# Performance work log

Hardware: AMD Instinct MI355X
Metric: run time of the kernel (lower is better)

Reference implementation:

```python
import jax, jax.numpy as jnp
import numpy as np
import math

B, S, E, H = 2, 2048, 1024, 16
D = E // H
EPS = 1e-5


def setup_inputs() -> dict:
    key = jax.random.key(0)
    ks = jax.random.split(key, 6)
    s = 1.0 / math.sqrt(E)
    return {
        "query": jax.random.normal(ks[0], (B, S, E), jnp.float32),
        "Wq": jax.random.normal(ks[1], (E, E), jnp.float32) * s,
        "bq": jnp.zeros((E,), jnp.float32),
        "Wk": jax.random.normal(ks[2], (E, E), jnp.float32) * s,
        "bk": jnp.zeros((E,), jnp.float32),
        "Wv": jax.random.normal(ks[3], (E, E), jnp.float32) * s,
        "bv": jnp.zeros((E,), jnp.float32),
        "Wo": jax.random.normal(ks[4], (E, E), jnp.float32) * s,
        "bo": jnp.zeros((E,), jnp.float32),
        "alpha": jnp.ones((1,), jnp.float32),
    }


def reference(query, Wq, bq, Wk, bk, Wv, bv, Wo, bo, alpha):
    # Q/K/V projections (nn.Linear: x @ W.T + b)
    q = (query @ Wq.T + bq).reshape(B, S, H, D)
    k = (query @ Wk.T + bk).reshape(B, S, H, D)
    v = (query @ Wv.T + bv).reshape(B, S, H, D)

    # YAT scores: (q.k)^2 / (||q-k||^2 + eps)
    qk = jnp.einsum('bqhd,bkhd->bhqk', q, k)          # [B,H,S,S]
    sq = jnp.einsum('bqhd,bqhd->bhq', q, q)           # ||q||^2
    sk = jnp.einsum('bkhd,bkhd->bhk', k, k)           # ||k||^2
    dist_sq = sq[..., :, None] + sk[..., None, :] - 2.0 * qk
    scores = (qk * qk) / (dist_sq + EPS)

    # learnable alpha scaling: scores * (sqrt(d)/log(1+d))^alpha
    scale = (jnp.sqrt(jnp.float32(D)) / jnp.log1p(jnp.float32(D))) ** alpha[0]
    scores = scores * scale

    attn = jax.nn.softmax(scores, axis=-1)
    out = jnp.einsum('bhqk,bkhd->bqhd', attn, v).reshape(B, S, E)
    return out @ Wo.T + bo
```

## Files before the change

### kernel.cpp

```cpp
#include <hip/hip_runtime.h>
#include <math.h>

#define BB 2
#define SS 2048
#define EE 1024
#define HH 16
#define DD 64
#define YAT_EPS 1e-5f

typedef __attribute__((ext_vector_type(8))) short bf16x8;
typedef __attribute__((ext_vector_type(4))) short short4v;
typedef __attribute__((ext_vector_type(4))) float f32x4;
typedef __attribute__((ext_vector_type(2))) float f32x2;
#define MFMA16(a, b, c) __builtin_amdgcn_mfma_f32_16x16x32_bf16((a), (b), (c), 0, 0, 0)

#if __has_builtin(__builtin_amdgcn_exp2f)
#define EXP2(x) __builtin_amdgcn_exp2f(x)
#else
#define EXP2(x) exp2f(x)
#endif
#if __has_builtin(__builtin_amdgcn_rcpf)
#define RCPF(x) __builtin_amdgcn_rcpf(x)
#else
#define RCPF(x) (1.0f / (x))
#endif

__device__ __forceinline__ unsigned short f2bf(float x) {
    unsigned int u = __float_as_uint(x);
    u += 0x7FFFu + ((u >> 16) & 1u);
    return (unsigned short)(u >> 16);
}
__device__ __forceinline__ float bf2f(unsigned short h) {
    return __uint_as_float(((unsigned int)h) << 16);
}
__device__ __forceinline__ short f2bf_t(float x) {
    return (short)(__float_as_uint(x) >> 16);
}

__device__ __forceinline__ void async_ld16(void* lds, const void* g) {
    __builtin_amdgcn_global_load_lds(
        (const __attribute__((address_space(1))) unsigned int*)g,
        (__attribute__((address_space(3))) unsigned int*)lds, 16, 0, 0);
}

__global__ __launch_bounds__(256) void split_f32(const float* __restrict__ in,
                                                 unsigned short* __restrict__ hi,
                                                 unsigned short* __restrict__ lo,
                                                 int n4) {
    int i = blockIdx.x * 256 + threadIdx.x;
    if (i >= n4) return;
    float4 v = ((const float4*)in)[i];
    ushort4 h, l;
    h.x = f2bf(v.x); l.x = f2bf(v.x - bf2f(h.x));
    h.y = f2bf(v.y); l.y = f2bf(v.y - bf2f(h.y));
    h.z = f2bf(v.z); l.z = f2bf(v.z - bf2f(h.z));
    h.w = f2bf(v.w); l.w = f2bf(v.w - bf2f(h.w));
    ((ushort4*)hi)[i] = h;
    ((ushort4*)lo)[i] = l;
}

__global__ __launch_bounds__(256) void split_w4(
        const float* __restrict__ Wq, const float* __restrict__ Wk,
        const float* __restrict__ Wv, const float* __restrict__ Wo,
        unsigned short* __restrict__ Whi, unsigned short* __restrict__ Wlo,
        unsigned short* __restrict__ Wohi) {
    int i = blockIdx.x * 256 + threadIdx.x;
    int y = blockIdx.y;
    const float* src = y == 0 ? Wq : y == 1 ? Wk : y == 2 ? Wv : Wo;
    unsigned short* hi = y < 3 ? Whi + (size_t)y * EE * EE : Wohi;
    float4 v = ((const float4*)src)[i];
    ushort4 h;
    h.x = f2bf(v.x); h.y = f2bf(v.y); h.z = f2bf(v.z); h.w = f2bf(v.w);
    ((ushort4*)hi)[i] = h;
    if (y < 2) {
        unsigned short* lo = Wlo + (size_t)y * EE * EE;
        ushort4 l;
        l.x = f2bf(v.x - bf2f(h.x));
        l.y = f2bf(v.y - bf2f(h.y));
        l.z = f2bf(v.z - bf2f(h.z));
        l.w = f2bf(v.w - bf2f(h.w));
        ((ushort4*)lo)[i] = l;
    }
}

template <int MODE, int PASSES>
__global__ __launch_bounds__(256, 2) void gemm3p(
        const unsigned short* __restrict__ Ahi, const unsigned short* __restrict__ Alo,
        const unsigned short* __restrict__ Bhi, const unsigned short* __restrict__ Blo,
        const float* __restrict__ bq, const float* __restrict__ bk,
        const float* __restrict__ bv,
        float* __restrict__ Cf,
        unsigned short* __restrict__ qhi, unsigned short* __restrict__ qlo,
        unsigned short* __restrict__ khi,
        unsigned short* __restrict__ v_sd,
        float* __restrict__ sqn, float* __restrict__ skn,
        int M, int N, int K) {
    __shared__ __align__(16) unsigned short LA_hi[128 * 32];
    __shared__ __align__(16) unsigned short LA_lo[128 * 32];
    __shared__ __align__(16) unsigned short LB_hi[128 * 32];
    __shared__ __align__(16) unsigned short LB_lo[128 * 32];

    const int t = threadIdx.x;
    const int w = t >> 6, lane = t & 63;
    const int quad = lane >> 4, lr = lane & 15;
    const int wy = w & 1, wx = w >> 1;
    const int m0 = blockIdx.y * 128, n0 = blockIdx.x * 128;

    const unsigned short* gsrc = nullptr;
    unsigned short* ldst = nullptr;
    if (w == 0)      { gsrc = Ahi + (size_t)m0 * K; ldst = LA_hi; }
    else if (w == 2) { gsrc = Bhi + (size_t)n0 * K; ldst = LB_hi; }
    else if (PASSES == 3 && w == 1) { gsrc = Alo + (size_t)m0 * K; ldst = LA_lo; }
    else if (PASSES == 3 && w == 3) { gsrc = Blo + (size_t)n0 * K; ldst = LB_lo; }
    const unsigned short* gl = gsrc ? gsrc + (size_t)(lane >> 2) * K + (lane & 3) * 8
                                    : nullptr;

    f32x4 acc[4][4];
    #pragma unroll
    for (int i = 0; i < 4; ++i)
        #pragma unroll
        for (int j = 0; j < 4; ++j)
            acc[i][j] = (f32x4){0.f, 0.f, 0.f, 0.f};

    for (int k0 = 0; k0 < K; k0 += 32) {
        __syncthreads();
        if (gl) {
            #pragma unroll
            for (int i = 0; i < 8; ++i)
                async_ld16(ldst + i * 512, gl + (size_t)i * 16 * K + k0);
        }
        __syncthreads();
        bf16x8 ah[4], al[4], bh_[4], bl_[4];
        #pragma unroll
        for (int i = 0; i < 4; ++i) {
            ah[i]  = *(const bf16x8*)&LA_hi[(wy * 64 + i * 16 + lr) * 32 + quad * 8];
            bh_[i] = *(const bf16x8*)&LB_hi[(wx * 64 + i * 16 + lr) * 32 + quad * 8];
            if (PASSES == 3) {
                al[i]  = *(const bf16x8*)&LA_lo[(wy * 64 + i * 16 + lr) * 32 + quad * 8];
                bl_[i] = *(const bf16x8*)&LB_lo[(wx * 64 + i * 16 + lr) * 32 + quad * 8];
            }
        }
        #pragma unroll
        for (int mg = 0; mg < 4; ++mg)
            #pragma unroll
            for (int ns = 0; ns < 4; ++ns) {
                f32x4 a = acc[mg][ns];
                a = MFMA16(ah[mg], bh_[ns], a);
                if (PASSES == 3) {
                    a = MFMA16(ah[mg], bl_[ns], a);
                    a = MFMA16(al[mg], bh_[ns], a);
                }
                acc[mg][ns] = a;
            }
    }

    const int ng = n0 + wx * 64;
    if (MODE == 0) {
        float bias_v[4];
        #pragma unroll
        for (int ns = 0; ns < 4; ++ns) bias_v[ns] = bq[ng + ns * 16 + lr];
        #pragma unroll
        for (int mg = 0; mg < 4; ++mg)
            #pragma unroll
            for (int r = 0; r < 4; ++r) {
                int m = m0 + wy * 64 + mg * 16 + quad * 4 + r;
                #pragma unroll
                for (int ns = 0; ns < 4; ++ns)
                    Cf[(size_t)m * N + ng + ns * 16 + lr] = acc[mg][ns][r] + bias_v[ns];
            }
    } else {
        const int path = MODE == 1 ? (ng >> 10) : 2;
        const int c = MODE == 1 ? (ng & 1023) : ng;
        const int h = c >> 6;
        const float* bias = path == 0 ? bq : path == 1 ? bk : bv;
        unsigned short* hi_p = path == 0 ? qhi : path == 1 ? khi : v_sd;
        float* nrm = path == 0 ? sqn : skn;
        float bias_v[4];
        #pragma unroll
        for (int ns = 0; ns < 4; ++ns) bias_v[ns] = bias[c + ns * 16 + lr];
        #pragma unroll
        for (int mg = 0; mg < 4; ++mg)
            #pragma unroll
            for (int r = 0; r < 4; ++r) {
                int m = m0 + wy * 64 + mg * 16 + quad * 4 + r;
                int b = m >> 11, s = m & (SS - 1);
                size_t base = ((size_t)(b * HH + h) * SS + s) * DD;
                float v4[4];
                #pragma unroll
                for (int ns = 0; ns < 4; ++ns) v4[ns] = acc[mg][ns][r] + bias_v[ns];
                if (path < 2) {
                    float pn = v4[0] * v4[0] + v4[1] * v4[1] + v4[2] * v4[2] + v4[3] * v4[3];
                    #pragma unroll
                    for (int off = 1; off < 16; off <<= 1) pn += __shfl_xor(pn, off);
                    if (lr == 0) nrm[(size_t)(b * HH + h) * SS + s] = pn;
                    #pragma unroll
                    for (int ns = 0; ns < 4; ++ns) {
                        unsigned short hv = f2bf(v4[ns]);
                        hi_p[base + ns * 16 + lr] = hv;
                        if (path == 0)
                            qlo[base + ns * 16 + lr] = f2bf(v4[ns] - bf2f(hv));
                    }
                } else {
                    #pragma unroll
                    for (int ns = 0; ns < 4; ++ns)
                        hi_p[base + ns * 16 + lr] = f2bf(v4[ns]);
                }
            }
    }
}

__global__ __launch_bounds__(256) void transpose_v(const unsigned short* __restrict__ v_sd,
                                                   unsigned short* __restrict__ vt) {
    __shared__ unsigned short T[64][65];
    const int t = threadIdx.x;
    const int bh = blockIdx.y, s0 = blockIdx.x * 64;
    {
        int sl = t >> 2, d4 = (t & 3) * 16;
        const unsigned short* src = &v_sd[((size_t)bh * SS + s0 + sl) * DD + d4];
        bf16x8 a = *(const bf16x8*)src;
        bf16x8 b = *(const bf16x8*)(src + 8);
        #pragma unroll
        for (int j = 0; j < 8; ++j) {
            T[sl][d4 + j] = (unsigned short)a[j];
            T[sl][d4 + 8 + j] = (unsigned short)b[j];
        }
    }
    __syncthreads();
    {
        int dl = t >> 2, s4 = (t & 3) * 16;
        bf16x8 a, b;
        #pragma unroll
        for (int j = 0; j < 8; ++j) {
            a[j] = (short)T[s4 + j][dl];
            b[j] = (short)T[s4 + 8 + j][dl];
        }
        unsigned short* dst = &vt[((size_t)bh * DD + dl) * SS + s0 + s4];
        *(bf16x8*)dst = a;
        *(bf16x8*)(dst + 8) = b;
    }
}

__global__ __launch_bounds__(256, 3) void yat_attn_mfma(
        const unsigned short* __restrict__ qhi, const unsigned short* __restrict__ qlo,
        const unsigned short* __restrict__ khi,
        const unsigned short* __restrict__ vt,
        const float* __restrict__ sqn, const float* __restrict__ skn,
        const float* __restrict__ alphap,
        unsigned short* __restrict__ ctxhi) {
    __shared__ __align__(16) unsigned short Ks[2][4096];
    __shared__ __align__(16) unsigned short Ps[2][4][16 * 68];

    const int t = threadIdx.x;
    const int w = t >> 6, lane = t & 63;
    const int quad = lane >> 4, lr = lane & 15;
    const int qt = blockIdx.x, bh = blockIdx.y;
    const int b = bh >> 4, h = bh & 15;
    const int row0 = qt * 64 + w * 16;
    const float cscale = powf(sqrtf((float)DD) / log1pf((float)DD), alphap[0])
                         * 1.4426950408889634f;

    bf16x8 qh[2], ql[2];
    #pragma unroll
    for (int kd = 0; kd < 2; ++kd) {
        size_t o = ((size_t)bh * SS + row0 + lr) * DD + kd * 32 + quad * 8;
        qh[kd] = *(const bf16x8*)&qhi[o];
        ql[kd] = *(const bf16x8*)&qlo[o];
    }
    const float sqe = sqn[(size_t)bh * SS + row0 + lr] + YAT_EPS;

    const int lrow = lane >> 3;
    const int lofs = lrow * 64 + (((lane & 7) ^ (lrow & 7)) << 3);
    const int sw = lr & 7;

    float m_r = -INFINITY, l_r = 0.f;
    f32x4 O[4];
    #pragma unroll
    for (int nd = 0; nd < 4; ++nd) O[nd] = (f32x4){0.f, 0.f, 0.f, 0.f};

    const size_t khi_base = (size_t)bh * SS * 64 + (size_t)w * 16 * 64 + lofs;
    const size_t skn_base = (size_t)bh * SS + quad * 4;

    {
        #pragma unroll
        for (int i2 = 0; i2 < 2; ++i2)
            async_ld16(&Ks[0][w * 1024 + i2 * 512], khi + khi_base + i2 * 512);
    }

    for (int it = 0; it < SS / 64; ++it) {
        const int p = it & 1;
        __syncthreads();
        if (it + 1 < SS / 64) {
            const size_t gb = khi_base + (size_t)(it + 1) * 64 * 64;
            #pragma unroll
            for (int i2 = 0; i2 < 2; ++i2)
                async_ld16(&Ks[p ^ 1][w * 1024 + i2 * 512], khi + gb + i2 * 512);
        }
        f32x4 acc[4];
        f32x4 sk4[4];
        const unsigned short* kb = Ks[p];
        #pragma unroll
        for (int st = 0; st < 4; ++st) {
            const int rbase = (st * 16 + lr) * 64;
            bf16x8 kh0 = *(const bf16x8*)&kb[rbase + ((quad    ) ^ sw) * 8];
            bf16x8 kh1 = *(const bf16x8*)&kb[rbase + ((quad + 4) ^ sw) * 8];
            sk4[st] = *(const f32x4*)&skn[skn_base + it * 64 + st * 16];
            f32x4 a = (f32x4){0.f, 0.f, 0.f, 0.f};
            a = MFMA16(kh0, qh[0], a);
            a = MFMA16(kh1, qh[1], a);
            a = MFMA16(kh0, ql[0], a);
            a = MFMA16(kh1, ql[1], a);
            acc[st] = a;
        }
        bf16x8 vf[4][2];
        #pragma unroll
        for (int nd = 0; nd < 4; ++nd)
            #pragma unroll
            for (int kk = 0; kk < 2; ++kk)
                vf[nd][kk] = *(const bf16x8*)&vt[((size_t)bh * DD + nd * 16 + lr) * SS
                                                 + it * 64 + kk * 32 + quad * 8];
        f32x2 U[8];
        const f32x2 sq2 = (f32x2){sqe, sqe};
        float mx = -INFINITY;
        #pragma unroll
        for (int st = 0; st < 4; ++st)
            #pragma unroll
            for (int pr = 0; pr < 2; ++pr) {
                f32x2 qk = (f32x2){acc[st][pr * 2], acc[st][pr * 2 + 1]};
                f32x2 skp = (f32x2){sk4[st][pr * 2], sk4[st][pr * 2 + 1]};
                f32x2 dd = sq2 + skp - (qk + qk);
                f32x2 rr = (f32x2){RCPF(dd.x), RCPF(dd.y)};
                f32x2 uu = qk * qk * rr;
                U[st * 2 + pr] = uu;
                mx = fmaxf(mx, fmaxf(uu.x, uu.y));
            }
        mx = fmaxf(mx, __shfl_xor(mx, 16));
        mx = fmaxf(mx, __shfl_xor(mx, 32));
        float mnew = fmaxf(m_r, mx);
        float cm = cscale * mnew;
        float aa = EXP2(__builtin_fmaf(cscale, m_r, -cm));
        m_r = mnew;
        unsigned short* myP = Ps[p][w];
        float rs = 0.f;
        #pragma unroll
        for (int st = 0; st < 4; ++st) {
            float e0 = EXP2(__builtin_fmaf(cscale, U[st * 2].x,     -cm));
            float e1 = EXP2(__builtin_fmaf(cscale, U[st * 2].y,     -cm));
            float e2 = EXP2(__builtin_fmaf(cscale, U[st * 2 + 1].x, -cm));
            float e3 = EXP2(__builtin_fmaf(cscale, U[st * 2 + 1].y, -cm));
            rs += (e0 + e1) + (e2 + e3);
            short4v pv;
            pv[0] = f2bf_t(e0); pv[1] = f2bf_t(e1);
            pv[2] = f2bf_t(e2); pv[3] = f2bf_t(e3);
            *(short4v*)&myP[lr * 68 + st * 16 + quad * 4] = pv;
        }
        rs += __shfl_xor(rs, 16);
        rs += __shfl_xor(rs, 32);
        l_r = l_r * aa + rs;
        float al_[4];
        #pragma unroll
        for (int r = 0; r < 4; ++r) al_[r] = __shfl(aa, quad * 4 + r);
        #pragma unroll
        for (int nd = 0; nd < 4; ++nd)
            #pragma unroll
            for (int r = 0; r < 4; ++r)
                O[nd][r] *= al_[r];
        bf16x8 pf[2];
        #pragma unroll
        for (int kk = 0; kk < 2; ++kk)
            pf[kk] = *(const bf16x8*)&myP[lr * 68 + kk * 32 + quad * 8];
        #pragma unroll
        for (int nd = 0; nd < 4; ++nd)
            #pragma unroll
            for (int kk = 0; kk < 2; ++kk)
                O[nd] = MFMA16(pf[kk], vf[nd][kk], O[nd]);
    }
    float linv[4];
    #pragma unroll
    for (int r = 0; r < 4; ++r) linv[r] = RCPF(__shfl(l_r, quad * 4 + r));
    #pragma unroll
    for (int r = 0; r < 4; ++r) {
        int row = row0 + quad * 4 + r;
        #pragma unroll
        for (int nd = 0; nd < 4; ++nd)
            ctxhi[((size_t)b * SS + row) * EE + h * DD + nd * 16 + lr] =
                f2bf(O[nd][r] * linv[r]);
    }
}

extern "C" void kernel_launch(void* const* d_in, const int* in_sizes, int n_in,
                              void* d_out, int out_size, void* d_ws, size_t ws_size,
                              hipStream_t stream) {
    const float* x     = (const float*)d_in[0];
    const float* Wq    = (const float*)d_in[1];
    const float* bq    = (const float*)d_in[2];
    const float* Wk    = (const float*)d_in[3];
    const float* bk    = (const float*)d_in[4];
    const float* Wv    = (const float*)d_in[5];
    const float* bv    = (const float*)d_in[6];
    const float* Wo    = (const float*)d_in[7];
    const float* bo    = (const float*)d_in[8];
    const float* alpha = (const float*)d_in[9];
    float* out = (float*)d_out;
    char* ws = (char*)d_ws;

    const int M = BB * SS;
    const size_t MB = 1u << 20;
    unsigned short* xhi  = (unsigned short*)(ws + 0 * MB);
    unsigned short* xlo  = (unsigned short*)(ws + 8 * MB);
    unsigned short* Whi  = (unsigned short*)(ws + 16 * MB);
    unsigned short* Wlo  = (unsigned short*)(ws + 22 * MB);
    unsigned short* vt   = (unsigned short*)(ws + 16 * MB);
    unsigned short* Wohi = (unsigned short*)(ws + 28 * MB);
    unsigned short* qhi  = (unsigned short*)(ws + 32 * MB);
    unsigned short* qlo  = (unsigned short*)(ws + 40 * MB);
    unsigned short* khi  = (unsigned short*)(ws + 48 * MB);
    unsigned short* v_sd = (unsigned short*)(ws + 64 * MB);
    float* sqn = (float*)(ws + 80 * MB);
    float* skn = (float*)(ws + 80 * MB + 256 * 1024);
    unsigned short* ctxhi = xhi;

    const int nX = M * EE / 4, nW = EE * EE / 4;
    split_f32<<<nX / 256, 256, 0, stream>>>(x, xhi, xlo, nX);
    split_w4<<<dim3(nW / 256, 4), 256, 0, stream>>>(Wq, Wk, Wv, Wo, Whi, Wlo, Wohi);

    gemm3p<1, 3><<<dim3(2 * EE / 128, M / 128), 256, 0, stream>>>(
        xhi, xlo, Whi, Wlo, bq, bk, nullptr, nullptr,
        qhi, qlo, khi, nullptr, sqn, skn, M, 2 * EE, EE);
    gemm3p<2, 1><<<dim3(EE / 128, M / 128), 256, 0, stream>>>(
        xhi, nullptr, Whi + 2 * (size_t)EE * EE, nullptr, nullptr, nullptr, bv, nullptr,
        nullptr, nullptr, nullptr, v_sd, nullptr, nullptr, M, EE, EE);

    transpose_v<<<dim3(SS / 64, BB * HH), 256, 0, stream>>>(v_sd, vt);

    yat_attn_mfma<<<dim3(SS / 64, BB * HH), 256, 0, stream>>>(
        qhi, qlo, khi, vt, sqn, skn, alpha, ctxhi);

    gemm3p<0, 1><<<dim3(EE / 128, M / 128), 256, 0, stream>>>(
        ctxhi, nullptr, Wohi, nullptr, bo, nullptr, nullptr, out,
        nullptr, nullptr, nullptr, nullptr, nullptr, nullptr, M, EE, EE);
}
```

Before: 384.3 us.

## Load K fragments directly from global memory, drop LDS double buffer and barriers

```diff
diff --git a/kernel.cpp b/kernel.cpp
--- a/kernel.cpp
+++ b/kernel.cpp
@@ -11,7 +11,6 @@
 typedef __attribute__((ext_vector_type(8))) short bf16x8;
 typedef __attribute__((ext_vector_type(4))) short short4v;
 typedef __attribute__((ext_vector_type(4))) float f32x4;
-typedef __attribute__((ext_vector_type(2))) float f32x2;
 #define MFMA16(a, b, c) __builtin_amdgcn_mfma_f32_16x16x32_bf16((a), (b), (c), 0, 0, 0)
 
 #if __has_builtin(__builtin_amdgcn_exp2f)
@@ -240,15 +239,14 @@
     }
 }
 
-__global__ __launch_bounds__(256, 3) void yat_attn_mfma(
+__global__ __launch_bounds__(256, 4) void yat_attn_mfma(
         const unsigned short* __restrict__ qhi, const unsigned short* __restrict__ qlo,
         const unsigned short* __restrict__ khi,
         const unsigned short* __restrict__ vt,
         const float* __restrict__ sqn, const float* __restrict__ skn,
         const float* __restrict__ alphap,
         unsigned short* __restrict__ ctxhi) {
-    __shared__ __align__(16) unsigned short Ks[2][4096];
-    __shared__ __align__(16) unsigned short Ps[2][4][16 * 68];
+    __shared__ __align__(16) unsigned short Ps[4][16 * 68];
 
     const int t = threadIdx.x;
     const int w = t >> 6, lane = t & 63;
@@ -268,42 +266,25 @@
     }
     const float sqe = sqn[(size_t)bh * SS + row0 + lr] + YAT_EPS;
 
-    const int lrow = lane >> 3;
-    const int lofs = lrow * 64 + (((lane & 7) ^ (lrow & 7)) << 3);
-    const int sw = lr & 7;
-
     float m_r = -INFINITY, l_r = 0.f;
     f32x4 O[4];
     #pragma unroll
     for (int nd = 0; nd < 4; ++nd) O[nd] = (f32x4){0.f, 0.f, 0.f, 0.f};
 
-    const size_t khi_base = (size_t)bh * SS * 64 + (size_t)w * 16 * 64 + lofs;
+    unsigned short* myP = Ps[w];
+    const size_t kfrag_base = (size_t)bh * SS * DD + (size_t)lr * DD + quad * 8;
     const size_t skn_base = (size_t)bh * SS + quad * 4;
 
-    {
-        #pragma unroll
-        for (int i2 = 0; i2 < 2; ++i2)
-            async_ld16(&Ks[0][w * 1024 + i2 * 512], khi + khi_base + i2 * 512);
-    }
-
     for (int it = 0; it < SS / 64; ++it) {
-        const int p = it & 1;
-        __syncthreads();
-        if (it + 1 < SS / 64) {
-            const size_t gb = khi_base + (size_t)(it + 1) * 64 * 64;
-            #pragma unroll
-            for (int i2 = 0; i2 < 2; ++i2)
-                async_ld16(&Ks[p ^ 1][w * 1024 + i2 * 512], khi + gb + i2 * 512);
-        }
+        const int kbase = it * 64;
         f32x4 acc[4];
         f32x4 sk4[4];
-        const unsigned short* kb = Ks[p];
         #pragma unroll
         for (int st = 0; st < 4; ++st) {
-            const int rbase = (st * 16 + lr) * 64;
-            bf16x8 kh0 = *(const bf16x8*)&kb[rbase + ((quad    ) ^ sw) * 8];
-            bf16x8 kh1 = *(const bf16x8*)&kb[rbase + ((quad + 4) ^ sw) * 8];
-            sk4[st] = *(const f32x4*)&skn[skn_base + it * 64 + st * 16];
+            size_t o = kfrag_base + (size_t)(kbase + st * 16) * DD;
+            bf16x8 kh0 = *(const bf16x8*)&khi[o];
+            bf16x8 kh1 = *(const bf16x8*)&khi[o + 32];
+            sk4[st] = *(const f32x4*)&skn[skn_base + kbase + st * 16];
             f32x4 a = (f32x4){0.f, 0.f, 0.f, 0.f};
             a = MFMA16(kh0, qh[0], a);
             a = MFMA16(kh1, qh[1], a);
@@ -317,21 +298,17 @@
             #pragma unroll
             for (int kk = 0; kk < 2; ++kk)
                 vf[nd][kk] = *(const bf16x8*)&vt[((size_t)bh * DD + nd * 16 + lr) * SS
-                                                 + it * 64 + kk * 32 + quad * 8];
-        f32x2 U[8];
-        const f32x2 sq2 = (f32x2){sqe, sqe};
+                                                 + kbase + kk * 32 + quad * 8];
         float mx = -INFINITY;
         #pragma unroll
         for (int st = 0; st < 4; ++st)
             #pragma unroll
-            for (int pr = 0; pr < 2; ++pr) {
-                f32x2 qk = (f32x2){acc[st][pr * 2], acc[st][pr * 2 + 1]};
-                f32x2 skp = (f32x2){sk4[st][pr * 2], sk4[st][pr * 2 + 1]};
-                f32x2 dd = sq2 + skp - (qk + qk);
-                f32x2 rr = (f32x2){RCPF(dd.x), RCPF(dd.y)};
-                f32x2 uu = qk * qk * rr;
-                U[st * 2 + pr] = uu;
-                mx = fmaxf(mx, fmaxf(uu.x, uu.y));
+            for (int r = 0; r < 4; ++r) {
+                float qk = acc[st][r];
+                float d = sqe + sk4[st][r] - 2.f * qk;
+                float u = qk * qk * RCPF(d);
+                acc[st][r] = u;
+                mx = fmaxf(mx, u);
             }
         mx = fmaxf(mx, __shfl_xor(mx, 16));
         mx = fmaxf(mx, __shfl_xor(mx, 32));
@@ -339,14 +316,13 @@
         float cm = cscale * mnew;
         float aa = EXP2(__builtin_fmaf(cscale, m_r, -cm));
         m_r = mnew;
-        unsigned short* myP = Ps[p][w];
         float rs = 0.f;
         #pragma unroll
         for (int st = 0; st < 4; ++st) {
-            float e0 = EXP2(__builtin_fmaf(cscale, U[st * 2].x,     -cm));
-            float e1 = EXP2(__builtin_fmaf(cscale, U[st * 2].y,     -cm));
-            float e2 = EXP2(__builtin_fmaf(cscale, U[st * 2 + 1].x, -cm));
-            float e3 = EXP2(__builtin_fmaf(cscale, U[st * 2 + 1].y, -cm));
+            float e0 = EXP2(__builtin_fmaf(cscale, acc[st][0], -cm));
+            float e1 = EXP2(__builtin_fmaf(cscale, acc[st][1], -cm));
+            float e2 = EXP2(__builtin_fmaf(cscale, acc[st][2], -cm));
+            float e3 = EXP2(__builtin_fmaf(cscale, acc[st][3], -cm));
             rs += (e0 + e1) + (e2 + e3);
             short4v pv;
             pv[0] = f2bf_t(e0); pv[1] = f2bf_t(e1);
```

New measurement: 444.0 us. 15.5% more time.
